# Kernel optimization log

Measured on AMD Instinct MI355X. Metric: run time of the kernel, lower is better.

The kernel has to match this reference:

```python
import jax, jax.numpy as jnp
import numpy as np

N = 4096            # data_length
T_IN, D_IN = 64, 128
F = 32 * 64         # target_length * output_dim


def setup_inputs() -> dict:
    key = jax.random.key(0)
    k1, k2, k3, k4 = jax.random.split(key, 4)
    xs = jax.random.normal(k1, (N, T_IN, D_IN), dtype=jnp.float32)
    W = jax.random.normal(k2, (T_IN * D_IN, F), dtype=jnp.float32) / np.sqrt(T_IN * D_IN)
    ys = jax.random.randint(k3, (N,), 0, 2, dtype=jnp.int32)  # {0,1} -> mapped to +-1 labels
    alphas = jax.random.normal(k4, (N,), dtype=jnp.float32)
    return {"xs": xs, "W": W, "ys": ys, "alphas": alphas}


def reference(xs, W, ys, alphas):
    gamma = 1.0 / F  # RBF bandwidth
    # encoder (stand-in for seq2seq): [N, T*D] @ [T*D, F] -> [N, F]
    X = xs.reshape(N, -1) @ W
    # pairwise squared distances via gram trick
    sq = jnp.sum(X * X, axis=-1)                       # [N]
    d2 = sq[:, None] + sq[None, :] - 2.0 * (X @ X.T)   # [N, N]
    d2 = jnp.maximum(d2, 0.0)
    K = jnp.exp(-gamma * d2)                           # RBF kernel matrix
    lab = (2 * ys - 1).astype(X.dtype)                 # +-1 labels
    G = (lab[:, None] * lab[None, :]) * K              # gram[i][j] = y_i y_j k(x_i, x_j)
    # 0.5 * alpha^T G alpha - sum(alpha)
    value = 0.5 * jnp.dot(alphas, G @ alphas) - jnp.sum(alphas)
    return value.reshape(1, 1)
```

## Files before the change

kernel.cpp:

```cpp
#include <hip/hip_runtime.h>
#include <hip/hip_bf16.h>

#define N_ROWS 4096
#define K_IN   8192
#define F_DIM  2048
#define GAMMA  (1.0f / 2048.0f)

typedef unsigned short u16;
typedef unsigned int   u32;
typedef unsigned char  u8;
typedef __attribute__((ext_vector_type(4))) int   i32x4;
typedef __attribute__((ext_vector_type(8))) int   i32x8;
typedef __attribute__((ext_vector_type(4))) float f32x4;
typedef __attribute__((ext_vector_type(2))) float f32x2;


__device__ __forceinline__ u32 pk4_fp8(float a, float b, float c, float d) {
  u32 u = 0;
  u = __builtin_amdgcn_cvt_pk_fp8_f32(a, b, u, false);
  u = __builtin_amdgcn_cvt_pk_fp8_f32(c, d, u, true);
  return u;
}
__device__ __forceinline__ u8 f8(float v) {
  return (u8)(__builtin_amdgcn_cvt_pk_fp8_f32(v, v, 0, false) & 0xff);
}

__device__ __forceinline__ void async16(const void* g, void* l) {
  __builtin_amdgcn_global_load_lds(
      (const __attribute__((address_space(1))) void*)g,
      (__attribute__((address_space(3))) void*)l, 16, 0, 0);
}


__global__ void convert_xs(const float* __restrict__ xs, u8* __restrict__ out) {
  __shared__ float t16[16][132];
  const int bid = blockIdx.x;
  const int rt = bid >> 6, kt = bid & 63;
  const int tid = threadIdx.x;
  const float* src = xs + (size_t)rt * 16 * K_IN + kt * 128;
#pragma unroll
  for (int j = 0; j < 2; ++j) {
    int i = tid + j * 256;
    int row = i >> 5, c4 = (i & 31) << 2;
    float4 v = *(const float4*)(src + (size_t)row * K_IN + c4);
    t16[row][c4 + 0] = v.x; t16[row][c4 + 1] = v.y;
    t16[row][c4 + 2] = v.z; t16[row][c4 + 3] = v.w;
  }
  __syncthreads();
  const int cw = tid >> 1, part = tid & 1;
  const int h = cw >> 6, l = cw & 63, q = l >> 4, rr = l & 15;
  const float* p = &t16[rr][q * 32 + h * 16 + part * 8];
  u32 u0 = pk4_fp8(p[0], p[1], p[2], p[3]);
  u32 u1 = pk4_fp8(p[4], p[5], p[6], p[7]);
  uint2 st = {u0, u1};
  *(uint2*)(out + ((size_t)(rt * 64 + kt) << 11) + cw * 16 + part * 8) = st;
}

__global__ void transpose_w(const float* __restrict__ W, u8* __restrict__ Wt) {
  __shared__ float tile[128][33];
  int k0 = blockIdx.x * 128;
  int f0 = blockIdx.y * 32;
  int tx = threadIdx.x, ty = threadIdx.y;
#pragma unroll
  for (int kk = 0; kk < 16; ++kk) {
    int k = kk * 8 + ty;
    tile[k][tx] = 64.0f * W[(size_t)(k0 + k) * F_DIM + f0 + tx];
  }
  __syncthreads();
  const int kt = k0 >> 7;
#pragma unroll
  for (int ff = 0; ff < 4; ++ff) {
    int f = ff * 8 + ty;
    int kk = tx * 4;
    u32 p = pk4_fp8(tile[kk][f], tile[kk + 1][f], tile[kk + 2][f], tile[kk + 3][f]);
    int rt = (f0 + f) >> 4, rr = (f0 + f) & 15;
    int q = kk >> 5, hh = (kk >> 4) & 1, b = kk & 15;
    *(u32*)(Wt + ((size_t)(rt * 64 + kt) << 11) + hh * 1024 + (q * 16 + rr) * 16 + b) = p;
  }
}

__global__ void prep(const float* __restrict__ alphas, const int* __restrict__ ys,
                     float* __restrict__ beta, float* __restrict__ out) {
  __shared__ float red[1024];
  int t = threadIdx.x;
  float s = 0.f;
  for (int i = t; i < N_ROWS; i += 1024) {
    float a = alphas[i];
    beta[i] = a * (float)(2 * ys[i] - 1);
    s += a;
  }
  red[t] = s;
  __syncthreads();
  for (int off = 512; off; off >>= 1) {
    if (t < off) red[t] += red[t + off];
    __syncthreads();
  }
  if (t == 0) out[0] = -red[0];
}

__global__ void row_sq(const u32* __restrict__ X, float* __restrict__ sq) {
  int wave = threadIdx.x >> 6, lane = threadIdx.x & 63;
  int row = blockIdx.x * 4 + wave;
  const u8* base = (const u8*)X + ((size_t)(row >> 4) << 15);
  const int rr = row & 15;
  float s = 0.f;
#pragma unroll
  for (int it = 0; it < 2; ++it) {
    int c = lane + it * 64;
    int kt = c >> 3, q = (c >> 1) & 3, h = c & 1;
    uint4 v = *(const uint4*)(base + kt * 2048 + h * 1024 + (q * 16 + rr) * 16);
    u32 w[4] = {v.x, v.y, v.z, v.w};
#pragma unroll
    for (int p = 0; p < 4; ++p) {
      f32x2 lo = __builtin_amdgcn_cvt_pk_f32_fp8(w[p], false);
      f32x2 hi = __builtin_amdgcn_cvt_pk_f32_fp8(w[p], true);
      s += lo[0] * lo[0] + lo[1] * lo[1] + hi[0] * hi[0] + hi[1] * hi[1];
    }
  }
#pragma unroll
  for (int off = 32; off; off >>= 1) s += __shfl_down(s, off);
  if (lane == 0) sq[row] = s;
}

__global__ __launch_bounds__(512, 2) void gemm_xw(const u8* __restrict__ A,
                                                  const u8* __restrict__ Bt,
                                                  u8* __restrict__ X) {
  __shared__ __align__(16) u8 smem[131072];
  const int tid = threadIdx.x;
  const int wg = blockIdx.x;
  const int L = (wg & 7) * 32 + (wg >> 3);
  const int m0 = (L & 15) << 8;
  const int n0 = (L >> 4) << 7;

  const int lane = tid & 63;
  const int wave = tid >> 6;
  const int kh = wave >> 2;
  const int w2 = wave & 3;
  const int wm = (w2 >> 1) << 7;
  const int wn = (w2 & 1) << 6;
  const int t = tid & 255;

  u8* sA  = smem + kh * 65536;
  u8* sB0 = sA + 32768;
  u8* sB1 = sB0 + 16384;

  const u8* pA = A  + (size_t)((m0 >> 4) + (t >> 7)) * 131072 + (t & 127) * 16;
  const u8* pB = Bt + (size_t)((n0 >> 4) + (t >> 7)) * 131072 + (t & 127) * 16;
  const int oT = t * 16;

  f32x4 acc[8][4];
  const f32x4 zero = {0.f, 0.f, 0.f, 0.f};
#pragma unroll
  for (int i = 0; i < 8; ++i)
#pragma unroll
    for (int j = 0; j < 4; ++j) acc[i][j] = zero;

#define STAGE_A(KT) { _Pragma("unroll") for (int j_ = 0; j_ < 8; ++j_) \
    async16(pA + (size_t)j_ * 262144 + (size_t)(KT) * 2048, sA + oT + j_ * 4096); }
#define STAGE_B(BUF, KT) { _Pragma("unroll") for (int j_ = 0; j_ < 4; ++j_) \
    async16(pB + (size_t)j_ * 262144 + (size_t)(KT) * 2048, (BUF) + oT + j_ * 4096); }
#define MFMA1(MT, NT, AF, BG) \
    acc[MT][NT] = __builtin_amdgcn_mfma_scale_f32_16x16x128_f8f6f4( \
        AF, BG, acc[MT][NT], 0, 0, 0, 127, 0, 121);

  const int kbase = kh * 32;
  STAGE_A(kbase)
  STAGE_B(sB0, kbase)
  __syncthreads();

  const int aB = lane * 16;
  const int sa0 = wm >> 4;
  const int sb0i = wn >> 4;

  for (int it = 0; it < 32; ++it) {
    const int kt = kbase + it;
    u8* sBc = (it & 1) ? sB1 : sB0;
    u8* sBn = (it & 1) ? sB0 : sB1;

    i32x8 af[8];
#pragma unroll
    for (int mt = 0; mt < 8; ++mt) {
      const u8* b_ = sA + (sa0 + mt) * 2048 + aB;
      i32x4 lo = *(const i32x4*)(b_);
      i32x4 hi = *(const i32x4*)(b_ + 1024);
      af[mt] = (i32x8){lo[0], lo[1], lo[2], lo[3], hi[0], hi[1], hi[2], hi[3]};
    }
    __syncthreads();

    if (it < 31) { STAGE_A(kt + 1) STAGE_B(sBn, kt + 1) }
#pragma unroll
    for (int nt = 0; nt < 4; ++nt) {
      const u8* b_ = sBc + (sb0i + nt) * 2048 + aB;
      i32x4 lo = *(const i32x4*)(b_);
      i32x4 hi = *(const i32x4*)(b_ + 1024);
      i32x8 bg = (i32x8){lo[0], lo[1], lo[2], lo[3], hi[0], hi[1], hi[2], hi[3]};
      MFMA1(0, nt, af[0], bg) MFMA1(1, nt, af[1], bg)
      MFMA1(2, nt, af[2], bg) MFMA1(3, nt, af[3], bg)
      MFMA1(4, nt, af[4], bg) MFMA1(5, nt, af[5], bg)
      MFMA1(6, nt, af[6], bg) MFMA1(7, nt, af[7], bg)
    }
    __syncthreads();
  }
#undef STAGE_A
#undef STAGE_B
#undef MFMA1

  __syncthreads();
  float* red = (float*)smem;
  if (kh == 1) {
#pragma unroll
    for (int mt = 0; mt < 8; ++mt)
#pragma unroll
      for (int nt = 0; nt < 4; ++nt)
        *(f32x4*)(red + ((size_t)t * 32 + mt * 4 + nt) * 4) = acc[mt][nt];
  }
  __syncthreads();
  if (kh == 0) {
    const int q = lane >> 4, r = lane & 15;
    const int qq0 = wn >> 5;
#pragma unroll
    for (int mt = 0; mt < 8; ++mt) {
#pragma unroll
      for (int nt = 0; nt < 4; ++nt) {
        f32x4 v = acc[mt][nt] + *(const f32x4*)(red + ((size_t)t * 32 + mt * 4 + nt) * 4);
        const int rt = (m0 >> 4) + (wm >> 4) + mt;
        const int qq = qq0 + (nt >> 1);
        const int hh = nt & 1;
        u8* dst = X + (size_t)rt * 32768 + (size_t)(n0 >> 7) * 2048 + hh * 1024 + r;
#pragma unroll
        for (int e = 0; e < 4; ++e)
          dst[(qq * 16 + ((q << 2) + e)) * 16] = f8(v[e]);
      }
    }
  }
}

__device__ __forceinline__ void gemm_tile_x(const u8* __restrict__ X, int m0, int n0,
                                            u8* sA, u8* sB, int tid, f32x4 acc[4][4]) {
  const int lane = tid & 63;
  const int wave = tid >> 6;
  const f32x4 zero = {0.f, 0.f, 0.f, 0.f};
#pragma unroll
  for (int mt = 0; mt < 4; ++mt)
#pragma unroll
    for (int nt = 0; nt < 4; ++nt) acc[mt][nt] = zero;

  const u8* pA = X + (size_t)((m0 >> 4) + (tid >> 7)) * 32768 + (tid & 127) * 16;
  const u8* pB = X + (size_t)((n0 >> 4) + (tid >> 7)) * 32768 + (tid & 127) * 16;
  const int oT = tid * 16;
  const int aB = lane * 16;
  const int sa0 = (wave >> 1) * 4, sb0 = (wave & 1) * 4;

  for (int kt = 0; kt < 16; ++kt) {
#pragma unroll
    for (int j = 0; j < 4; ++j) {
      async16(pA + (size_t)j * 65536 + kt * 2048, sA + oT + j * 4096);
      async16(pB + (size_t)j * 65536 + kt * 2048, sB + oT + j * 4096);
    }
    __syncthreads();

    i32x8 af[4], bg[4];
#pragma unroll
    for (int mt = 0; mt < 4; ++mt) {
      const u8* b_ = sA + (sa0 + mt) * 2048 + aB;
      i32x4 lo = *(const i32x4*)(b_);
      i32x4 hi = *(const i32x4*)(b_ + 1024);
      af[mt] = (i32x8){lo[0], lo[1], lo[2], lo[3], hi[0], hi[1], hi[2], hi[3]};
    }
#pragma unroll
    for (int nt = 0; nt < 4; ++nt) {
      const u8* b_ = sB + (sb0 + nt) * 2048 + aB;
      i32x4 lo = *(const i32x4*)(b_);
      i32x4 hi = *(const i32x4*)(b_ + 1024);
      bg[nt] = (i32x8){lo[0], lo[1], lo[2], lo[3], hi[0], hi[1], hi[2], hi[3]};
    }
#pragma unroll
    for (int mt = 0; mt < 4; ++mt)
#pragma unroll
      for (int nt = 0; nt < 4; ++nt)
        acc[mt][nt] = __builtin_amdgcn_mfma_scale_f32_16x16x128_f8f6f4(
            af[mt], bg[nt], acc[mt][nt], 0, 0, 0, 127, 0, 127);
    __syncthreads();
  }
}

__global__ __launch_bounds__(256, 3) void gemm_kern(const u8* __restrict__ X,
                                                    const float* __restrict__ sq,
                                                    const float* __restrict__ beta,
                                                    float* __restrict__ out) {
  __shared__ __align__(16) u8 sA[128 * 128];
  __shared__ __align__(16) u8 sB[128 * 128];
  const int tid = threadIdx.x;
  int bid = blockIdx.x;
  int ib = 0;
  while (bid >= 32 - ib) { bid -= 32 - ib; ++ib; }
  const int jb = ib + bid;
  const int m0 = ib << 7;
  const int n0 = jb << 7;

  f32x4 acc[4][4];
  gemm_tile_x(X, m0, n0, sA, sB, tid, acc);

  const int lane = tid & 63;
  const int q = lane >> 4;
  const int r = lane & 15;
  const int wave = tid >> 6;
  const int wm = (wave >> 1) << 6;
  const int wn = (wave & 1) << 6;

  float sqj[4], bj[4];
#pragma unroll
  for (int nt = 0; nt < 4; ++nt) {
    int j = n0 + wn + (nt << 4) + r;
    sqj[nt] = sq[j];
    bj[nt] = beta[j];
  }
  float local = 0.f;
#pragma unroll
  for (int mt = 0; mt < 4; ++mt) {
#pragma unroll
    for (int e = 0; e < 4; ++e) {
      int i = m0 + wm + (mt << 4) + (q << 2) + e;
      float sqi = sq[i];
      float bi = beta[i];
#pragma unroll
      for (int nt = 0; nt < 4; ++nt) {
        float d2 = fmaxf(sqi + sqj[nt] - 2.f * acc[mt][nt][e], 0.f);
        local += bi * bj[nt] * __expf(-GAMMA * d2);
      }
    }
  }
  local *= (ib == jb) ? 0.5f : 1.0f;
#pragma unroll
  for (int off = 32; off; off >>= 1) local += __shfl_down(local, off);
  if (lane == 0) atomicAdd(out, local);
}


extern "C" void kernel_launch(void* const* d_in, const int* in_sizes, int n_in,
                              void* d_out, int out_size, void* d_ws, size_t ws_size,
                              hipStream_t stream) {
  const float* xs = (const float*)d_in[0];
  const float* W = (const float*)d_in[1];
  const int* ys = (const int*)d_in[2];
  const float* alphas = (const float*)d_in[3];
  float* out = (float*)d_out;

  char* ws = (char*)d_ws;
  u8* xs_f8 = (u8*)ws;
  u8* Wt_f8 = (u8*)(ws + 33554432);
  u8* X_f8  = (u8*)(ws + 50331648);
  float* sq   = (float*)(ws + 58720256);
  float* beta = (float*)(ws + 58736640);

  convert_xs<<<16384, 256, 0, stream>>>(xs, xs_f8);
  dim3 tb(32, 8);
  dim3 tg(K_IN / 128, F_DIM / 32);
  transpose_w<<<tg, tb, 0, stream>>>(W, Wt_f8);
  prep<<<1, 1024, 0, stream>>>(alphas, ys, beta, out);

  gemm_xw<<<256, 512, 0, stream>>>(xs_f8, Wt_f8, X_f8);
  row_sq<<<N_ROWS / 4, 256, 0, stream>>>((const u32*)X_f8, sq);
  gemm_kern<<<528, 256, 0, stream>>>(X_f8, sq, beta, out);
}
```

Before: 358.8 us.

## Pipeline XW GEMM with triple buffering, double-buffer Gram GEMM, coalesce W transpose

The XW GEMM drops its split-K layout, where two wave halves reduced partial sums through shared memory. It becomes a 256x128 tile with 8 waves, each computing 64x64, fed by a 3-stage async shared-memory ring with explicit vmcnt waits and raw barriers. The Gram GEMM tile loop is double-buffered so the next k-tile loads while MFMAs run, and MFMA sections are wrapped in raised wave priority. The W transpose now stages packed fp8 words in shared memory and writes 16-byte coalesced stores. The cost is lower occupancy from fewer blocks per CU and more shared memory per block, and the hand-written waitcnt counts must match the number of async loads issued.

```diff
diff --git a/kernel.cpp b/kernel.cpp
--- a/kernel.cpp
+++ b/kernel.cpp
@@ -58,6 +58,7 @@
 
 __global__ void transpose_w(const float* __restrict__ W, u8* __restrict__ Wt) {
   __shared__ float tile[128][33];
+  __shared__ u32 ob[1024];
   int k0 = blockIdx.x * 128;
   int f0 = blockIdx.y * 32;
   int tx = threadIdx.x, ty = threadIdx.y;
@@ -67,16 +68,20 @@
     tile[k][tx] = 64.0f * W[(size_t)(k0 + k) * F_DIM + f0 + tx];
   }
   __syncthreads();
-  const int kt = k0 >> 7;
 #pragma unroll
   for (int ff = 0; ff < 4; ++ff) {
     int f = ff * 8 + ty;
     int kk = tx * 4;
     u32 p = pk4_fp8(tile[kk][f], tile[kk + 1][f], tile[kk + 2][f], tile[kk + 3][f]);
-    int rt = (f0 + f) >> 4, rr = (f0 + f) & 15;
-    int q = kk >> 5, hh = (kk >> 4) & 1, b = kk & 15;
-    *(u32*)(Wt + ((size_t)(rt * 64 + kt) << 11) + hh * 1024 + (q * 16 + rr) * 16 + b) = p;
-  }
+    int rtl = f >> 4, rr = f & 15;
+    int q = kk >> 5, hh = (kk >> 4) & 1;
+    ob[rtl * 512 + hh * 256 + (q * 16 + rr) * 4 + ((kk & 15) >> 2)] = p;
+  }
+  __syncthreads();
+  const int t = ty * 32 + tx;
+  const int kt = k0 >> 7, rt0 = f0 >> 4;
+  uint4* dst = (uint4*)(Wt + ((size_t)((rt0 + (t >> 7)) * 64 + kt) << 11));
+  dst[t & 127] = ((const uint4*)ob)[t];
 }
 
 __global__ void prep(const float* __restrict__ alphas, const int* __restrict__ ys,
@@ -122,10 +127,11 @@
   if (lane == 0) sq[row] = s;
 }
 
-__global__ __launch_bounds__(512, 2) void gemm_xw(const u8* __restrict__ A,
+__global__ __launch_bounds__(512, 1) void gemm_xw(const u8* __restrict__ A,
                                                   const u8* __restrict__ Bt,
                                                   u8* __restrict__ X) {
-  __shared__ __align__(16) u8 smem[131072];
+  __shared__ __align__(16) u8 sA[3][32768];
+  __shared__ __align__(16) u8 sB[3][16384];
   const int tid = threadIdx.x;
   const int wg = blockIdx.x;
   const int L = (wg & 7) * 32 + (wg >> 3);
@@ -134,109 +140,101 @@
 
   const int lane = tid & 63;
   const int wave = tid >> 6;
-  const int kh = wave >> 2;
-  const int w2 = wave & 3;
-  const int wm = (w2 >> 1) << 7;
-  const int wn = (w2 & 1) << 6;
-  const int t = tid & 255;
-
-  u8* sA  = smem + kh * 65536;
-  u8* sB0 = sA + 32768;
-  u8* sB1 = sB0 + 16384;
-
-  const u8* pA = A  + (size_t)((m0 >> 4) + (t >> 7)) * 131072 + (t & 127) * 16;
-  const u8* pB = Bt + (size_t)((n0 >> 4) + (t >> 7)) * 131072 + (t & 127) * 16;
-  const int oT = t * 16;
-
-  f32x4 acc[8][4];
+  const int wm = (wave >> 1) << 6;
+  const int wn = (wave & 1) << 6;
+
+  const u8* pA[4]; const u8* pB[2];
+#pragma unroll
+  for (int j = 0; j < 4; ++j)
+    pA[j] = A + (size_t)((m0 >> 4) + j * 4 + (tid >> 7)) * 131072 + (tid & 127) * 16;
+#pragma unroll
+  for (int j = 0; j < 2; ++j)
+    pB[j] = Bt + (size_t)((n0 >> 4) + j * 4 + (tid >> 7)) * 131072 + (tid & 127) * 16;
+  const int oT = (tid & 127) * 16 + ((tid >> 7) << 11);
+
+  f32x4 acc[4][4];
   const f32x4 zero = {0.f, 0.f, 0.f, 0.f};
 #pragma unroll
-  for (int i = 0; i < 8; ++i)
+  for (int i = 0; i < 4; ++i)
 #pragma unroll
     for (int j = 0; j < 4; ++j) acc[i][j] = zero;
 
-#define STAGE_A(KT) { _Pragma("unroll") for (int j_ = 0; j_ < 8; ++j_) \
-    async16(pA + (size_t)j_ * 262144 + (size_t)(KT) * 2048, sA + oT + j_ * 4096); }
-#define STAGE_B(BUF, KT) { _Pragma("unroll") for (int j_ = 0; j_ < 4; ++j_) \
-    async16(pB + (size_t)j_ * 262144 + (size_t)(KT) * 2048, (BUF) + oT + j_ * 4096); }
+#define STAGE(BUF, KT) { \
+    _Pragma("unroll") for (int j_ = 0; j_ < 4; ++j_) \
+      async16(pA[j_] + (size_t)(KT) * 2048, sA[BUF] + oT + j_ * 8192); \
+    _Pragma("unroll") for (int j_ = 0; j_ < 2; ++j_) \
+      async16(pB[j_] + (size_t)(KT) * 2048, sB[BUF] + oT + j_ * 8192); }
 #define MFMA1(MT, NT, AF, BG) \
     acc[MT][NT] = __builtin_amdgcn_mfma_scale_f32_16x16x128_f8f6f4( \
         AF, BG, acc[MT][NT], 0, 0, 0, 127, 0, 121);
 
-  const int kbase = kh * 32;
-  STAGE_A(kbase)
-  STAGE_B(sB0, kbase)
-  __syncthreads();
+  STAGE(0, 0)
+  STAGE(1, 1)
+  asm volatile("s_waitcnt vmcnt(6)" ::: "memory");
+  __builtin_amdgcn_s_barrier();
 
   const int aB = lane * 16;
   const int sa0 = wm >> 4;
-  const int sb0i = wn >> 4;
-
-  for (int it = 0; it < 32; ++it) {
-    const int kt = kbase + it;
-    u8* sBc = (it & 1) ? sB1 : sB0;
-    u8* sBn = (it & 1) ? sB0 : sB1;
-
-    i32x8 af[8];
-#pragma unroll
-    for (int mt = 0; mt < 8; ++mt) {
-      const u8* b_ = sA + (sa0 + mt) * 2048 + aB;
+  const int sb0 = wn >> 4;
+
+  int cur = 0, nb = 2;
+  for (int kt = 0; kt < 64; ++kt) {
+    const bool st = (kt + 2 < 64);
+    if (st) STAGE(nb, kt + 2)
+
+    i32x8 af[4], bg[4];
+#pragma unroll
+    for (int mt = 0; mt < 4; ++mt) {
+      const u8* b_ = sA[cur] + (sa0 + mt) * 2048 + aB;
       i32x4 lo = *(const i32x4*)(b_);
       i32x4 hi = *(const i32x4*)(b_ + 1024);
       af[mt] = (i32x8){lo[0], lo[1], lo[2], lo[3], hi[0], hi[1], hi[2], hi[3]};
     }
-    __syncthreads();
-
-    if (it < 31) { STAGE_A(kt + 1) STAGE_B(sBn, kt + 1) }
 #pragma unroll
     for (int nt = 0; nt < 4; ++nt) {
-      const u8* b_ = sBc + (sb0i + nt) * 2048 + aB;
+      const u8* b_ = sB[cur] + (sb0 + nt) * 2048 + aB;
       i32x4 lo = *(const i32x4*)(b_);
       i32x4 hi = *(const i32x4*)(b_ + 1024);
-      i32x8 bg = (i32x8){lo[0], lo[1], lo[2], lo[3], hi[0], hi[1], hi[2], hi[3]};
-      MFMA1(0, nt, af[0], bg) MFMA1(1, nt, af[1], bg)
-      MFMA1(2, nt, af[2], bg) MFMA1(3, nt, af[3], bg)
-      MFMA1(4, nt, af[4], bg) MFMA1(5, nt, af[5], bg)
-      MFMA1(6, nt, af[6], bg) MFMA1(7, nt, af[7], bg)
-    }
-    __syncthreads();
-  }
-#undef STAGE_A
-#undef STAGE_B
+      bg[nt] = (i32x8){lo[0], lo[1], lo[2], lo[3], hi[0], hi[1], hi[2], hi[3]};
+    }
+    __builtin_amdgcn_s_setprio(1);
+#pragma unroll
+    for (int mt = 0; mt < 4; ++mt)
+#pragma unroll
+      for (int nt = 0; nt < 4; ++nt)
+        MFMA1(mt, nt, af[mt], bg[nt])
+    __builtin_amdgcn_s_setprio(0);
+
+    if (st) {
+      asm volatile("s_waitcnt vmcnt(6)" ::: "memory");
+    } else if (kt < 63) {
+      asm volatile("s_waitcnt vmcnt(0)" ::: "memory");
+    }
+    __builtin_amdgcn_s_barrier();
+    cur = (cur == 2) ? 0 : cur + 1;
+    nb  = (nb == 2) ? 0 : nb + 1;
+  }
+#undef STAGE
 #undef MFMA1
 
-  __syncthreads();
-  float* red = (float*)smem;
-  if (kh == 1) {
-#pragma unroll
-    for (int mt = 0; mt < 8; ++mt)
-#pragma unroll
-      for (int nt = 0; nt < 4; ++nt)
-        *(f32x4*)(red + ((size_t)t * 32 + mt * 4 + nt) * 4) = acc[mt][nt];
-  }
-  __syncthreads();
-  if (kh == 0) {
-    const int q = lane >> 4, r = lane & 15;
-    const int qq0 = wn >> 5;
-#pragma unroll
-    for (int mt = 0; mt < 8; ++mt) {
-#pragma unroll
-      for (int nt = 0; nt < 4; ++nt) {
-        f32x4 v = acc[mt][nt] + *(const f32x4*)(red + ((size_t)t * 32 + mt * 4 + nt) * 4);
-        const int rt = (m0 >> 4) + (wm >> 4) + mt;
-        const int qq = qq0 + (nt >> 1);
-        const int hh = nt & 1;
-        u8* dst = X + (size_t)rt * 32768 + (size_t)(n0 >> 7) * 2048 + hh * 1024 + r;
-#pragma unroll
-        for (int e = 0; e < 4; ++e)
-          dst[(qq * 16 + ((q << 2) + e)) * 16] = f8(v[e]);
-      }
+  const int q = lane >> 4, r = lane & 15;
+#pragma unroll
+  for (int mt = 0; mt < 4; ++mt) {
+#pragma unroll
+    for (int nt = 0; nt < 4; ++nt) {
+      const int rt_x = ((m0 + wm) >> 4) + mt;
+      const int qx = (wn >> 5) + (nt >> 1);
+      u8* dst = X + (size_t)(rt_x * 16 + (n0 >> 7)) * 2048 + (nt & 1) * 1024 + r;
+#pragma unroll
+      for (int e = 0; e < 4; ++e)
+        dst[(qx * 16 + (q << 2) + e) * 16] = f8(acc[mt][nt][e]);
     }
   }
 }
 
 __device__ __forceinline__ void gemm_tile_x(const u8* __restrict__ X, int m0, int n0,
-                                            u8* sA, u8* sB, int tid, f32x4 acc[4][4]) {
+                                            u8 (*sA)[16384], u8 (*sB)[16384],
+                                            int tid, f32x4 acc[4][4]) {
   const int lane = tid & 63;
   const int wave = tid >> 6;
   const f32x4 zero = {0.f, 0.f, 0.f, 0.f};
@@ -251,45 +249,51 @@
   const int aB = lane * 16;
   const int sa0 = (wave >> 1) * 4, sb0 = (wave & 1) * 4;
 
+#define STG(KT, BUF) { _Pragma("unroll") for (int j_ = 0; j_ < 4; ++j_) { \
+    async16(pA + (size_t)j_ * 65536 + (size_t)(KT) * 2048, sA[BUF] + oT + j_ * 4096); \
+    async16(pB + (size_t)j_ * 65536 + (size_t)(KT) * 2048, sB[BUF] + oT + j_ * 4096); } }
+
+  STG(0, 0)
+  __syncthreads();
+
   for (int kt = 0; kt < 16; ++kt) {
-#pragma unroll
-    for (int j = 0; j < 4; ++j) {
-      async16(pA + (size_t)j * 65536 + kt * 2048, sA + oT + j * 4096);
-      async16(pB + (size_t)j * 65536 + kt * 2048, sB + oT + j * 4096);
-    }
-    __syncthreads();
+    const int cur = kt & 1, nxt = cur ^ 1;
+    if (kt < 15) STG(kt + 1, nxt)
 
     i32x8 af[4], bg[4];
 #pragma unroll
     for (int mt = 0; mt < 4; ++mt) {
-      const u8* b_ = sA + (sa0 + mt) * 2048 + aB;
+      const u8* b_ = sA[cur] + (sa0 + mt) * 2048 + aB;
       i32x4 lo = *(const i32x4*)(b_);
       i32x4 hi = *(const i32x4*)(b_ + 1024);
       af[mt] = (i32x8){lo[0], lo[1], lo[2], lo[3], hi[0], hi[1], hi[2], hi[3]};
     }
 #pragma unroll
     for (int nt = 0; nt < 4; ++nt) {
-      const u8* b_ = sB + (sb0 + nt) * 2048 + aB;
+      const u8* b_ = sB[cur] + (sb0 + nt) * 2048 + aB;
       i32x4 lo = *(const i32x4*)(b_);
       i32x4 hi = *(const i32x4*)(b_ + 1024);
       bg[nt] = (i32x8){lo[0], lo[1], lo[2], lo[3], hi[0], hi[1], hi[2], hi[3]};
     }
+    __builtin_amdgcn_s_setprio(1);
 #pragma unroll
     for (int mt = 0; mt < 4; ++mt)
 #pragma unroll
       for (int nt = 0; nt < 4; ++nt)
         acc[mt][nt] = __builtin_amdgcn_mfma_scale_f32_16x16x128_f8f6f4(
             af[mt], bg[nt], acc[mt][nt], 0, 0, 0, 127, 0, 127);
+    __builtin_amdgcn_s_setprio(0);
     __syncthreads();
   }
-}
-
-__global__ __launch_bounds__(256, 3) void gemm_kern(const u8* __restrict__ X,
+#undef STG
+}
+
+__global__ __launch_bounds__(256, 2) void gemm_kern(const u8* __restrict__ X,
                                                     const float* __restrict__ sq,
                                                     const float* __restrict__ beta,
                                                     float* __restrict__ out) {
-  __shared__ __align__(16) u8 sA[128 * 128];
-  __shared__ __align__(16) u8 sB[128 * 128];
+  __shared__ __align__(16) u8 sA[2][16384];
+  __shared__ __align__(16) u8 sB[2][16384];
   const int tid = threadIdx.x;
   int bid = blockIdx.x;
   int ib = 0;
```

Result: slower. 376.4 us (+4.9%).
